# Performance work log

Measured on AMD Instinct MI355X. Metric: run time of the kernel, lower is better.

## Reference

```python
import jax, jax.numpy as jnp
import numpy as np

B, CIN, COUT, N, K = 4, 64, 64, 16384, 8


def setup_inputs() -> dict:
    key = jax.random.key(0)
    k1, k2, k3, k4, k5 = jax.random.split(key, 5)
    features = jax.random.normal(k1, (B, CIN, N), dtype=jnp.float32)
    neighborhood = jax.random.randint(k2, (B, K, N), 0, N, dtype=jnp.int32)
    positions = jax.random.uniform(k3, (B, 3, N), dtype=jnp.float32)
    # learned parameters (kaiming-uniform-ish init)
    lim_t = np.sqrt(6.0 / CIN)
    weight_theta = jax.random.uniform(k4, (3, CIN, COUT), dtype=jnp.float32,
                                      minval=-lim_t, maxval=lim_t)
    weight_bias = jax.random.uniform(k5, (CIN, COUT), dtype=jnp.float32,
                                     minval=-lim_t, maxval=lim_t)
    bias = jnp.zeros((COUT,), dtype=jnp.float32)
    return {"features": features, "weight_theta": weight_theta,
            "weight_bias": weight_bias, "neighborhood": neighborhood,
            "positions": positions, "bias": bias}


def reference(features, weight_theta, weight_bias, neighborhood, positions, bias):
    # features: [B, Cin, N]; positions: [B, 3, N]; neighborhood: [B, K, N]
    Bv, Cin, Nv = features.shape
    Kv = neighborhood.shape[1]
    # gather neighbor positions: pos_j[b,d,k,n] = positions[b,d, nbh[b,k,n]]
    pos_j = jnp.take_along_axis(positions[:, :, None, :],
                                neighborhood[:, None, :, :].astype(jnp.int32),
                                axis=3)                        # [B,3,K,N]
    delta = pos_j - positions[:, :, None, :]                   # [B,3,K,N]
    # position-dependent linear weight applied to center features:
    # contrib[b,k,o,n] = sum_d delta[b,d,k,n] * (theta.f)[b,d,o,n] + (wb.f)[b,o,n]
    ft = jnp.einsum('dio,bin->bdon', weight_theta, features)   # [B,3,Cout,N]
    fb = jnp.einsum('io,bin->bon', weight_bias, features)      # [B,Cout,N]
    contrib = jnp.einsum('bdkn,bdon->bkon', delta, ft) + fb[:, None]  # [B,K,Cout,N]

    def scatter_b(contrib_b, idx_b):
        # contrib_b: [K,Cout,N], idx_b: [K,N]
        data = contrib_b.transpose(0, 2, 1).reshape(-1, contrib_b.shape[1])  # [K*N, Cout]
        ids = idx_b.reshape(-1)
        return jax.ops.segment_sum(data, ids, num_segments=Nv).T  # [Cout, N]

    out = jax.vmap(scatter_b)(contrib, neighborhood)           # [B,Cout,N]
    return out + bias[None, :, None]
```

## Files before the change

### kernel.cpp

```cpp
#include <hip/hip_runtime.h>
#include <hip/hip_fp16.h>

#define B_    4
#define CIN_  64
#define COUT_ 64
#define N_    16384
#define K_    8
#define CAP_  16

#define EDGES_PER_B (K_ * N_)
#define TOT_EDGES   (B_ * EDGES_PER_B)


__device__ __forceinline__ unsigned pack_h2(float a, float b) {
    return (unsigned)__half_as_ushort(__float2half(a))
         | ((unsigned)__half_as_ushort(__float2half(b)) << 16);
}

__device__ __forceinline__ float edge_dot(uint2 v, float qx, float qy, float qz) {
    const float f0 = __half2float(__ushort_as_half((unsigned short)(v.x)));
    const float f1 = __half2float(__ushort_as_half((unsigned short)(v.x >> 16)));
    const float f2 = __half2float(__ushort_as_half((unsigned short)(v.y)));
    const float f3 = __half2float(__ushort_as_half((unsigned short)(v.y >> 16)));
    return fmaf(qx, f0, fmaf(qy, f1, fmaf(qz, f2, f3)));
}

__global__ __launch_bounds__(512, 4) void fc_contribD(
    const float* __restrict__ feat,
    const float* __restrict__ theta,
    const float* __restrict__ wbias,
    const int*   __restrict__ nbh,
    const float* __restrict__ pos,
    int*         __restrict__ cursor,
    int*         __restrict__ bucket,
    uint2*       __restrict__ ftfb,
    float*       __restrict__ ws2)
{
    __shared__ float4 Wl[CIN_ * COUT_];
    __shared__ float  Fl[CIN_ * 64];

    const int tid  = threadIdx.x;
    const int lane = tid & 63;
    const int w    = tid >> 6;

    const int blocks_per_b = N_ / 128;
    const int b     = blockIdx.x / blocks_per_b;
    const int nbase = (blockIdx.x % blocks_per_b) * 128;

    for (int e = tid; e < CIN_ * COUT_; e += 512) {
        const int i = e >> 6, o = e & 63;
        float4 wv;
        wv.x = theta[0 * CIN_ * COUT_ + i * COUT_ + o];
        wv.y = theta[1 * CIN_ * COUT_ + i * COUT_ + o];
        wv.z = theta[2 * CIN_ * COUT_ + i * COUT_ + o];
        wv.w = wbias[i * COUT_ + o];
        Wl[e] = wv;
    }

    const float* featb = feat + (size_t)b * CIN_ * N_;
    const float* posb  = pos  + (size_t)b * 3 * N_;
    const int*   nbhb  = nbh  + (size_t)b * K_ * N_;
    int*         curb  = cursor + b * N_;
    int*         bkb   = bucket + (size_t)b * N_ * CAP_;
    uint2*       fbb   = ftfb + ((size_t)b * N_ << 6);
    float*       ws2b  = ws2 + ((size_t)b * N_ << 6);

    for (int t = 0; t < 2; ++t) {
        const int n0 = nbase + t * 64;
        const int nn = w * 8;

        __syncthreads();
        for (int r = 0; r < 8; ++r) {
            const int i = r * 8 + w;
            Fl[i * 64 + lane] = featb[(size_t)i * N_ + n0 + lane];
        }

        const int pe = lane >> 3;
        const int ke = lane & 7;
        const int ne = n0 + nn + pe;
        const int je = nbhb[ke * N_ + ne];
        const int sle = atomicAdd(&curb[je], 1);
        if (sle < CAP_) bkb[je * CAP_ + sle] = ne;

        __syncthreads();

        float4 acc[8];
        #pragma unroll
        for (int j = 0; j < 8; ++j) acc[j] = make_float4(0.f, 0.f, 0.f, 0.f);

        #pragma unroll 2
        for (int i = 0; i < CIN_; ++i) {
            const float4 wv = Wl[i * 64 + lane];
            const float4 fA = *(const float4*)&Fl[i * 64 + nn];
            const float4 fB = *(const float4*)&Fl[i * 64 + nn + 4];
            const float fs[8] = {fA.x, fA.y, fA.z, fA.w, fB.x, fB.y, fB.z, fB.w};
            #pragma unroll
            for (int j = 0; j < 8; ++j) {
                acc[j].x = fmaf(wv.x, fs[j], acc[j].x);
                acc[j].y = fmaf(wv.y, fs[j], acc[j].y);
                acc[j].z = fmaf(wv.z, fs[j], acc[j].z);
                acc[j].w = fmaf(wv.w, fs[j], acc[j].w);
            }
        }

        const unsigned long long ovf = __ballot(sle >= CAP_);

        #pragma unroll
        for (int p = 0; p < 8; ++p) {
            const int n = n0 + nn + p;
            const float px = posb[0 * N_ + n];
            const float py = posb[1 * N_ + n];
            const float pz = posb[2 * N_ + n];
            float4 a = acc[p];
            a.w = fmaf(-px, a.x, fmaf(-py, a.y, fmaf(-pz, a.z, a.w)));

            uint2 v;
            v.x = pack_h2(a.x, a.y);
            v.y = pack_h2(a.z, a.w);
            fbb[((size_t)n << 6) + lane] = v;

            const unsigned m8 = (unsigned)((ovf >> (p * 8)) & 0xFFull);
            if (m8) {
                #pragma unroll
                for (int k = 0; k < 8; ++k) {
                    if ((m8 >> k) & 1) {
                        const int src = p * 8 + k;
                        const int jt = __shfl(je, src);
                        const float qx = posb[jt];
                        const float qy = posb[N_ + jt];
                        const float qz = posb[2 * N_ + jt];
                        const float c = fmaf(qx, a.x,
                                        fmaf(qy, a.y,
                                        fmaf(qz, a.z, a.w)));
                        atomicAdd(&ws2b[((size_t)jt << 6) + lane], c);
                    }
                }
            }
        }
    }
}

__global__ __launch_bounds__(512, 8) void fc_gatherD(
    const uint2* __restrict__ ftfb,
    const int*   __restrict__ bucket,
    const int*   __restrict__ cursor,
    const float* __restrict__ ws2,
    const float* __restrict__ pos,
    const float* __restrict__ bias,
    float*       __restrict__ out)
{
    __shared__ float T[64][65];
    const int tid  = threadIdx.x;
    const int lane = tid & 63;
    const int w    = tid >> 6;

    const int tiles_per_b = N_ / 64;
    const int b  = blockIdx.x / tiles_per_b;
    const int n0 = (blockIdx.x % tiles_per_b) * 64;

    const uint2* fbb  = ftfb + ((size_t)b * N_ << 6);
    const int*   bkb  = bucket + (size_t)b * N_ * CAP_;
    const float* posb = pos + (size_t)b * 3 * N_;
    const float* ws2b = ws2 + ((size_t)b * N_ << 6);

    for (int g = 0; g < 8; ++g) {
        const int jj = w * 8 + g;
        const int j  = n0 + jj;
        const int cnt_tot = cursor[b * N_ + j];
        const int cnt = cnt_tot < CAP_ ? cnt_tot : CAP_;
        const float qx = posb[j];
        const float qy = posb[N_ + j];
        const float qz = posb[2 * N_ + j];

        const int myidx = (lane < cnt) ? bkb[j * CAP_ + lane] : 0;

        float acc = (cnt_tot > CAP_) ? ws2b[((size_t)j << 6) + lane] : 0.f;

        int e = 0;
        for (; e + 4 <= cnt; e += 4) {
            const int m0 = __shfl(myidx, e + 0);
            const int m1 = __shfl(myidx, e + 1);
            const int m2 = __shfl(myidx, e + 2);
            const int m3 = __shfl(myidx, e + 3);
            const uint2 v0 = fbb[((size_t)m0 << 6) + lane];
            const uint2 v1 = fbb[((size_t)m1 << 6) + lane];
            const uint2 v2 = fbb[((size_t)m2 << 6) + lane];
            const uint2 v3 = fbb[((size_t)m3 << 6) + lane];
            acc += edge_dot(v0, qx, qy, qz);
            acc += edge_dot(v1, qx, qy, qz);
            acc += edge_dot(v2, qx, qy, qz);
            acc += edge_dot(v3, qx, qy, qz);
        }
        for (; e < cnt; ++e) {
            const int m = __shfl(myidx, e);
            const uint2 v = fbb[((size_t)m << 6) + lane];
            acc += edge_dot(v, qx, qy, qz);
        }
        T[jj][lane] = acc;
    }
    __syncthreads();

    float* outb = out + (size_t)b * COUT_ * N_;
    for (int r = 0; r < 8; ++r) {
        const int o = r * 8 + w;
        outb[(size_t)o * N_ + n0 + lane] = T[lane][o] + bias[o];
    }
}

__global__ __launch_bounds__(256) void flexconv_main(
    const float* __restrict__ feat,
    const float* __restrict__ theta,
    const float* __restrict__ wbias,
    const int*   __restrict__ nbh,
    const float* __restrict__ pos,
    float*       __restrict__ ws)
{
    __shared__ float4 Wl[CIN_ * COUT_];
    __shared__ float  Fl[CIN_ * 64];

    const int tid  = threadIdx.x;
    const int lane = tid & 63;
    const int w    = tid >> 6;

    const int blocks_per_b = N_ / 128;
    const int b     = blockIdx.x / blocks_per_b;
    const int nbase = (blockIdx.x % blocks_per_b) * 128;

    for (int e = tid; e < CIN_ * COUT_; e += 256) {
        const int i = e >> 6, o = e & 63;
        float4 wv;
        wv.x = theta[0 * CIN_ * COUT_ + i * COUT_ + o];
        wv.y = theta[1 * CIN_ * COUT_ + i * COUT_ + o];
        wv.z = theta[2 * CIN_ * COUT_ + i * COUT_ + o];
        wv.w = wbias[i * COUT_ + o];
        Wl[e] = wv;
    }

    const float* featb = feat + (size_t)b * CIN_ * N_;
    const float* posb  = pos  + (size_t)b * 3 * N_;
    const int*   nbhb  = nbh  + (size_t)b * K_ * N_;
    float*       wsb   = ws   + (size_t)b * N_ * COUT_;

    for (int t = 0; t < 2; ++t) {
        const int n0 = nbase + t * 64;

        __syncthreads();
        for (int r = 0; r < 16; ++r) {
            const int i = r * 4 + w;
            Fl[i * 64 + lane] = featb[(size_t)i * N_ + n0 + lane];
        }
        __syncthreads();

        for (int g = 0; g < 4; ++g) {
            const int nn = w * 16 + g * 4;
            float4 acc[4];
            #pragma unroll
            for (int j = 0; j < 4; ++j) acc[j] = make_float4(0.f, 0.f, 0.f, 0.f);

            #pragma unroll 8
            for (int i = 0; i < CIN_; ++i) {
                const float4 wv = Wl[i * 64 + lane];
                const float f0 = Fl[i * 64 + nn + 0];
                const float f1 = Fl[i * 64 + nn + 1];
                const float f2 = Fl[i * 64 + nn + 2];
                const float f3 = Fl[i * 64 + nn + 3];
                acc[0].x = fmaf(wv.x, f0, acc[0].x);
                acc[0].y = fmaf(wv.y, f0, acc[0].y);
                acc[0].z = fmaf(wv.z, f0, acc[0].z);
                acc[0].w = fmaf(wv.w, f0, acc[0].w);
                acc[1].x = fmaf(wv.x, f1, acc[1].x);
                acc[1].y = fmaf(wv.y, f1, acc[1].y);
                acc[1].z = fmaf(wv.z, f1, acc[1].z);
                acc[1].w = fmaf(wv.w, f1, acc[1].w);
                acc[2].x = fmaf(wv.x, f2, acc[2].x);
                acc[2].y = fmaf(wv.y, f2, acc[2].y);
                acc[2].z = fmaf(wv.z, f2, acc[2].z);
                acc[2].w = fmaf(wv.w, f2, acc[2].w);
                acc[3].x = fmaf(wv.x, f3, acc[3].x);
                acc[3].y = fmaf(wv.y, f3, acc[3].y);
                acc[3].z = fmaf(wv.z, f3, acc[3].z);
                acc[3].w = fmaf(wv.w, f3, acc[3].w);
            }

            #pragma unroll
            for (int j = 0; j < 4; ++j) {
                const int n = n0 + nn + j;
                const float px = posb[0 * N_ + n];
                const float py = posb[1 * N_ + n];
                const float pz = posb[2 * N_ + n];
                const float4 a = acc[j];
                #pragma unroll
                for (int k = 0; k < K_; ++k) {
                    const int idx = nbhb[k * N_ + n];
                    const float dx = posb[0 * N_ + idx] - px;
                    const float dy = posb[1 * N_ + idx] - py;
                    const float dz = posb[2 * N_ + idx] - pz;
                    const float c  = fmaf(dx, a.x, fmaf(dy, a.y, fmaf(dz, a.z, a.w)));
                    atomicAdd(&wsb[(size_t)idx * COUT_ + lane], c);
                }
            }
        }
    }
}

__global__ __launch_bounds__(256) void flexconv_finish(
    const float* __restrict__ ws,
    const float* __restrict__ bias,
    float*       __restrict__ out)
{
    __shared__ float T[64][65];
    const int tid  = threadIdx.x;
    const int lane = tid & 63;
    const int w    = tid >> 6;

    const int tiles_per_b = N_ / 64;
    const int b  = blockIdx.x / tiles_per_b;
    const int n0 = (blockIdx.x % tiles_per_b) * 64;

    const float* wsb = ws + (size_t)b * N_ * COUT_;
    for (int r = 0; r < 16; ++r) {
        const int nn = r * 4 + w;
        T[nn][lane] = wsb[(size_t)(n0 + nn) * COUT_ + lane];
    }
    __syncthreads();

    float* outb = out + (size_t)b * COUT_ * N_;
    for (int r = 0; r < 16; ++r) {
        const int o = r * 4 + w;
        outb[(size_t)o * N_ + n0 + lane] = T[lane][o] + bias[o];
    }
}

extern "C" void kernel_launch(void* const* d_in, const int* in_sizes, int n_in,
                              void* d_out, int out_size, void* d_ws, size_t ws_size,
                              hipStream_t stream) {
    const float* features = (const float*)d_in[0];
    const float* theta    = (const float*)d_in[1];
    const float* wbias    = (const float*)d_in[2];
    const int*   nbh      = (const int*)  d_in[3];
    const float* pos      = (const float*)d_in[4];
    const float* bias     = (const float*)d_in[5];
    float* out = (float*)d_out;

    {
        const size_t ftfb_bytes   = ((size_t)B_ * N_ << 6) * sizeof(uint2);
        const size_t bucket_bytes = (size_t)B_ * N_ * CAP_ * sizeof(int);
        const size_t cursor_bytes = (size_t)B_ * N_ * sizeof(int);
        const size_t ws2_bytes    = ((size_t)B_ * N_ << 6) * sizeof(float);

        size_t off = 0;
        uint2* ftfb   = (uint2*)((char*)d_ws + off); off += ftfb_bytes;
        int*   bucket = (int*)  ((char*)d_ws + off); off += bucket_bytes;
        int*   cursor = (int*)  ((char*)d_ws + off); off += cursor_bytes;
        float* ws2    = (float*)((char*)d_ws + off); off += ws2_bytes;

        if (ws_size >= off) {
            hipMemsetAsync(cursor, 0, cursor_bytes + ws2_bytes, stream);
            fc_contribD<<<B_ * (N_ / 128), 512, 0, stream>>>(features, theta, wbias,
                                                             nbh, pos, cursor,
                                                             bucket, ftfb, ws2);
            fc_gatherD<<<B_ * (N_ / 64), 512, 0, stream>>>(ftfb, bucket, cursor,
                                                           ws2, pos, bias, out);
            return;
        }
    }

    {
        float* ws = (float*)d_ws;
        const size_t ws_bytes = (size_t)B_ * N_ * COUT_ * sizeof(float);
        hipMemsetAsync(ws, 0, ws_bytes, stream);
        flexconv_main<<<B_ * (N_ / 128), 256, 0, stream>>>(features, theta, wbias,
                                                           nbh, pos, ws);
        flexconv_finish<<<B_ * (N_ / 64), 256, 0, stream>>>(ws, bias, out);
    }
}
```

Measured before the change: 162.5 us.

## Precompute per-edge fp16 contributions in producer and reduce them directly in gather

The producer kernel now computes each edge's full contribution (target position dotted with the per-source features) and stores it as one fp16 value per channel per edge. Buckets hold edge ids instead of source ids. The gather kernel then just sums fp16 values instead of loading 4-half vectors and doing dot products. This cuts random gather traffic per edge from 512B to 128B rows, at the cost of a larger, edge-indexed intermediate buffer. It also adds random position reads in the producer and needs more workspace, which could trigger the fallback path if workspace is insufficient.

```diff
diff --git a/kernel.cpp b/kernel.cpp
--- a/kernel.cpp
+++ b/kernel.cpp
@@ -12,20 +12,7 @@
 #define TOT_EDGES   (B_ * EDGES_PER_B)
 
 
-__device__ __forceinline__ unsigned pack_h2(float a, float b) {
-    return (unsigned)__half_as_ushort(__float2half(a))
-         | ((unsigned)__half_as_ushort(__float2half(b)) << 16);
-}
-
-__device__ __forceinline__ float edge_dot(uint2 v, float qx, float qy, float qz) {
-    const float f0 = __half2float(__ushort_as_half((unsigned short)(v.x)));
-    const float f1 = __half2float(__ushort_as_half((unsigned short)(v.x >> 16)));
-    const float f2 = __half2float(__ushort_as_half((unsigned short)(v.y)));
-    const float f3 = __half2float(__ushort_as_half((unsigned short)(v.y >> 16)));
-    return fmaf(qx, f0, fmaf(qy, f1, fmaf(qz, f2, f3)));
-}
-
-__global__ __launch_bounds__(512, 4) void fc_contribD(
+__global__ __launch_bounds__(512, 4) void fc_contribE(
     const float* __restrict__ feat,
     const float* __restrict__ theta,
     const float* __restrict__ wbias,
@@ -33,7 +20,7 @@
     const float* __restrict__ pos,
     int*         __restrict__ cursor,
     int*         __restrict__ bucket,
-    uint2*       __restrict__ ftfb,
+    __half*      __restrict__ cval,
     float*       __restrict__ ws2)
 {
     __shared__ float4 Wl[CIN_ * COUT_];
@@ -62,7 +49,7 @@
     const int*   nbhb  = nbh  + (size_t)b * K_ * N_;
     int*         curb  = cursor + b * N_;
     int*         bkb   = bucket + (size_t)b * N_ * CAP_;
-    uint2*       fbb   = ftfb + ((size_t)b * N_ << 6);
+    __half*      cvb   = cval + ((size_t)b * EDGES_PER_B << 6);
     float*       ws2b  = ws2 + ((size_t)b * N_ << 6);
 
     for (int t = 0; t < 2; ++t) {
@@ -80,7 +67,7 @@
         const int ne = n0 + nn + pe;
         const int je = nbhb[ke * N_ + ne];
         const int sle = atomicAdd(&curb[je], 1);
-        if (sle < CAP_) bkb[je * CAP_ + sle] = ne;
+        if (sle < CAP_) bkb[je * CAP_ + sle] = ne * K_ + ke;
 
         __syncthreads();
 
@@ -114,40 +101,29 @@
             float4 a = acc[p];
             a.w = fmaf(-px, a.x, fmaf(-py, a.y, fmaf(-pz, a.z, a.w)));
 
-            uint2 v;
-            v.x = pack_h2(a.x, a.y);
-            v.y = pack_h2(a.z, a.w);
-            fbb[((size_t)n << 6) + lane] = v;
-
-            const unsigned m8 = (unsigned)((ovf >> (p * 8)) & 0xFFull);
-            if (m8) {
-                #pragma unroll
-                for (int k = 0; k < 8; ++k) {
-                    if ((m8 >> k) & 1) {
-                        const int src = p * 8 + k;
-                        const int jt = __shfl(je, src);
-                        const float qx = posb[jt];
-                        const float qy = posb[N_ + jt];
-                        const float qz = posb[2 * N_ + jt];
-                        const float c = fmaf(qx, a.x,
-                                        fmaf(qy, a.y,
-                                        fmaf(qz, a.z, a.w)));
-                        atomicAdd(&ws2b[((size_t)jt << 6) + lane], c);
-                    }
-                }
+            __half* crow = cvb + ((size_t)(n * K_) << 6) + lane;
+            #pragma unroll
+            for (int k = 0; k < K_; ++k) {
+                const int jt = nbhb[k * N_ + n];
+                const float qx = posb[jt];
+                const float qy = posb[N_ + jt];
+                const float qz = posb[2 * N_ + jt];
+                const float c  = fmaf(qx, a.x, fmaf(qy, a.y, fmaf(qz, a.z, a.w)));
+                crow[(size_t)k << 6] = __float2half(c);
+                if ((ovf >> (p * 8 + k)) & 1ull)
+                    atomicAdd(&ws2b[((size_t)jt << 6) + lane], c);
             }
         }
     }
 }
 
-__global__ __launch_bounds__(512, 8) void fc_gatherD(
-    const uint2* __restrict__ ftfb,
-    const int*   __restrict__ bucket,
-    const int*   __restrict__ cursor,
-    const float* __restrict__ ws2,
-    const float* __restrict__ pos,
-    const float* __restrict__ bias,
-    float*       __restrict__ out)
+__global__ __launch_bounds__(512, 8) void fc_gatherE(
+    const __half* __restrict__ cval,
+    const int*    __restrict__ bucket,
+    const int*    __restrict__ cursor,
+    const float*  __restrict__ ws2,
+    const float*  __restrict__ bias,
+    float*        __restrict__ out)
 {
     __shared__ float T[64][65];
     const int tid  = threadIdx.x;
@@ -158,19 +134,15 @@
     const int b  = blockIdx.x / tiles_per_b;
     const int n0 = (blockIdx.x % tiles_per_b) * 64;
 
-    const uint2* fbb  = ftfb + ((size_t)b * N_ << 6);
-    const int*   bkb  = bucket + (size_t)b * N_ * CAP_;
-    const float* posb = pos + (size_t)b * 3 * N_;
-    const float* ws2b = ws2 + ((size_t)b * N_ << 6);
+    const __half* cvb  = cval + ((size_t)b * EDGES_PER_B << 6);
+    const int*    bkb  = bucket + (size_t)b * N_ * CAP_;
+    const float*  ws2b = ws2 + ((size_t)b * N_ << 6);
 
     for (int g = 0; g < 8; ++g) {
         const int jj = w * 8 + g;
         const int j  = n0 + jj;
         const int cnt_tot = cursor[b * N_ + j];
         const int cnt = cnt_tot < CAP_ ? cnt_tot : CAP_;
-        const float qx = posb[j];
-        const float qy = posb[N_ + j];
-        const float qz = posb[2 * N_ + j];
 
         const int myidx = (lane < cnt) ? bkb[j * CAP_ + lane] : 0;
 
@@ -182,19 +154,15 @@
             const int m1 = __shfl(myidx, e + 1);
             const int m2 = __shfl(myidx, e + 2);
             const int m3 = __shfl(myidx, e + 3);
-            const uint2 v0 = fbb[((size_t)m0 << 6) + lane];
-            const uint2 v1 = fbb[((size_t)m1 << 6) + lane];
-            const uint2 v2 = fbb[((size_t)m2 << 6) + lane];
-            const uint2 v3 = fbb[((size_t)m3 << 6) + lane];
-            acc += edge_dot(v0, qx, qy, qz);
-            acc += edge_dot(v1, qx, qy, qz);
-            acc += edge_dot(v2, qx, qy, qz);
-            acc += edge_dot(v3, qx, qy, qz);
+            const float c0 = __half2float(cvb[((size_t)m0 << 6) + lane]);
+            const float c1 = __half2float(cvb[((size_t)m1 << 6) + lane]);
+            const float c2 = __half2float(cvb[((size_t)m2 << 6) + lane]);
+            const float c3 = __half2float(cvb[((size_t)m3 << 6) + lane]);
+            acc += (c0 + c1) + (c2 + c3);
         }
         for (; e < cnt; ++e) {
             const int m = __shfl(myidx, e);
-            const uint2 v = fbb[((size_t)m << 6) + lane];
-            acc += edge_dot(v, qx, qy, qz);
+            acc += __half2float(cvb[((size_t)m << 6) + lane]);
         }
         T[jj][lane] = acc;
     }
@@ -343,24 +311,24 @@
     float* out = (float*)d_out;
 
     {
-        const size_t ftfb_bytes   = ((size_t)B_ * N_ << 6) * sizeof(uint2);
+        const size_t cval_bytes   = ((size_t)TOT_EDGES << 6) * sizeof(__half);
         const size_t bucket_bytes = (size_t)B_ * N_ * CAP_ * sizeof(int);
         const size_t cursor_bytes = (size_t)B_ * N_ * sizeof(int);
         const size_t ws2_bytes    = ((size_t)B_ * N_ << 6) * sizeof(float);
 
         size_t off = 0;
-        uint2* ftfb   = (uint2*)((char*)d_ws + off); off += ftfb_bytes;
-        int*   bucket = (int*)  ((char*)d_ws + off); off += bucket_bytes;
-        int*   cursor = (int*)  ((char*)d_ws + off); off += cursor_bytes;
-        float* ws2    = (float*)((char*)d_ws + off); off += ws2_bytes;
+        __half* cval   = (__half*)((char*)d_ws + off); off += cval_bytes;
+        int*    bucket = (int*)   ((char*)d_ws + off); off += bucket_bytes;
+        int*    cursor = (int*)   ((char*)d_ws + off); off += cursor_bytes;
+        float*  ws2    = (float*) ((char*)d_ws + off); off += ws2_bytes;
 
         if (ws_size >= off) {
             hipMemsetAsync(cursor, 0, cursor_bytes + ws2_bytes, stream);
-            fc_contribD<<<B_ * (N_ / 128), 512, 0, stream>>>(features, theta, wbias,
+            fc_contribE<<<B_ * (N_ / 128), 512, 0, stream>>>(features, theta, wbias,
                                                              nbh, pos, cursor,
-                                                             bucket, ftfb, ws2);
-            fc_gatherD<<<B_ * (N_ / 64), 512, 0, stream>>>(ftfb, bucket, cursor,
-                                                           ws2, pos, bias, out);
+                                                             bucket, cval, ws2);
+            fc_gatherE<<<B_ * (N_ / 64), 512, 0, stream>>>(cval, bucket, cursor,
+                                                           ws2, bias, out);
             return;
         }
     }
```

Measured after the change: 178.6 us. 9.9% more time.
